# Optimization experiments

Hardware: AMD Instinct MI355X
Metric: run time of the kernel (lower is better)

Reference implementation:

```python
import jax, jax.numpy as jnp
import numpy as np

BATCH, T, VOCAB, HIDDEN = 32, 256, 8192, 1024
SCALE = 0.02  # small init so logits stay sane through the recurrence


def setup_inputs() -> dict:
    key = jax.random.key(0)
    ks = jax.random.split(key, 4)
    inputs = jax.random.normal(ks[0], (BATCH, T, VOCAB), dtype=jnp.float32)
    Wi = jax.random.normal(ks[1], (VOCAB, 4 * HIDDEN), dtype=jnp.float32) * SCALE
    Wh = jax.random.normal(ks[2], (HIDDEN, 4 * HIDDEN), dtype=jnp.float32) * SCALE
    bh = jnp.zeros((4 * HIDDEN,), dtype=jnp.float32)
    Wp = jax.random.normal(ks[3], (HIDDEN, VOCAB), dtype=jnp.float32) * SCALE
    bp = jnp.zeros((VOCAB,), dtype=jnp.float32)
    c0 = jnp.zeros((BATCH, HIDDEN), dtype=jnp.float32)
    h0 = jnp.zeros((BATCH, HIDDEN), dtype=jnp.float32)
    return {"inputs": inputs, "Wi": Wi, "Wh": Wh, "bh": bh,
            "Wp": Wp, "bp": bp, "c0": c0, "h0": h0}


def _decode(inputs, Wi, Wh, bh, Wp, bp, c0, h0, rng):
    vocab = inputs.shape[2]

    def step(carry, x_t):
        rng, c, h, last_pred = carry
        rng, cat_rng = jax.random.split(rng)
        x = last_pred  # teacher_force=False: feed back sampled one-hot token
        # fused LSTM gates (flax gate order i, f, g, o)
        z = x @ Wi + h @ Wh + bh  # [B, 4H]
        i, f, g, o = jnp.split(z, 4, axis=-1)
        c = jax.nn.sigmoid(f) * c + jax.nn.sigmoid(i) * jnp.tanh(g)
        h = jax.nn.sigmoid(o) * jnp.tanh(c)
        logits = h @ Wp + bp  # [B, V]
        tok = jax.random.categorical(cat_rng, logits)  # [B] int
        pred = jax.nn.one_hot(tok, vocab, dtype=jnp.float32)  # [B, V]
        return (rng, c, h, pred), (logits, pred)

    init = (rng, c0, h0, inputs[:, 0])
    xs = jnp.swapaxes(inputs, 0, 1)  # [T, B, V]
    _, (logits, preds) = jax.lax.scan(step, init, xs)
    # scan stacks on axis 0; original scan_in_dim puts time back on axis 1
    return jnp.swapaxes(logits, 0, 1), jnp.swapaxes(preds, 0, 1)


def reference(inputs, Wi, Wh, bh, Wp, bp, c0, h0):
    rng = jax.random.key(42)  # stands in for self.make_rng('lstm')
    return _decode(inputs, Wi, Wh, bh, Wp, bp, c0, h0, rng)
```

## Files before the change

### kernel.cpp

```cpp
#include <hip/hip_runtime.h>
#include <cstdint>
#include <cstddef>


namespace {

constexpr int BB = 32;
constexpr int TT = 256;
constexpr int VV = 8192;
constexpr int HH = 1024;
constexpr int ZC = 4096;
constexpr int NCOL = VV + ZC;
constexpr int SPL = 4;
constexpr int K0S = 8;

__host__ __device__ inline uint32_t rotl(uint32_t v, int r) {
  return (v << r) | (v >> (32 - r));
}

__host__ __device__ inline void tf2x32(uint32_t k0, uint32_t k1,
                                       uint32_t x0, uint32_t x1,
                                       uint32_t &o0, uint32_t &o1) {
  const uint32_t ks2 = k0 ^ k1 ^ 0x1BD11BDAu;
  x0 += k0; x1 += k1;
#define R4A { x0+=x1; x1=rotl(x1,13); x1^=x0; x0+=x1; x1=rotl(x1,15); x1^=x0; \
              x0+=x1; x1=rotl(x1,26); x1^=x0; x0+=x1; x1=rotl(x1, 6); x1^=x0; }
#define R4B { x0+=x1; x1=rotl(x1,17); x1^=x0; x0+=x1; x1=rotl(x1,29); x1^=x0; \
              x0+=x1; x1=rotl(x1,16); x1^=x0; x0+=x1; x1=rotl(x1,24); x1^=x0; }
  R4A; x0 += k1;  x1 += ks2 + 1u;
  R4B; x0 += ks2; x1 += k0 + 2u;
  R4A; x0 += k0;  x1 += k1 + 3u;
  R4B; x0 += k1;  x1 += ks2 + 4u;
  R4A; x0 += ks2; x1 += k0 + 5u;
#undef R4A
#undef R4B
  o0 = x0; o1 = x1;
}

__device__ inline float sigf(float x) { return 1.0f / (1.0f + expf(-x)); }

__global__ __launch_bounds__(256) void k0_partial(
    const float* __restrict__ inputs,
    const float* __restrict__ h0,
    const float* __restrict__ Wi,
    const float* __restrict__ Wh,
    float* __restrict__ zpart0)
{
  const int cb = blockIdx.x % (ZC / 64);
  const int s  = blockIdx.x / (ZC / 64);
  const int c  = threadIdx.x & 63;
  const int w  = threadIdx.x >> 6;
  const int col = cb * 64 + c;
  const int u0 = s * 1152 + w * 288;

  float acc[BB];
#pragma unroll
  for (int b = 0; b < BB; ++b) acc[b] = 0.0f;

  for (int ui = 0; ui < 288; ++ui) {
    const int u = u0 + ui;
    const float wv = (u < VV) ? Wi[(size_t)u * ZC + col]
                              : Wh[(size_t)(u - VV) * ZC + col];
#pragma unroll
    for (int b = 0; b < BB; ++b) {
      const float a = (u < VV) ? inputs[(size_t)b * TT * VV + u]
                               : h0[b * HH + (u - VV)];
      acc[b] = fmaf(a, wv, acc[b]);
    }
  }

  __shared__ float red[4][BB][64];
#pragma unroll
  for (int b = 0; b < BB; ++b) red[w][b][c] = acc[b];
  __syncthreads();
  for (int i = threadIdx.x; i < BB * 64; i += 256) {
    const int b = i >> 6, cc = i & 63;
    const float s4 = red[0][b][cc] + red[1][b][cc] + red[2][b][cc] + red[3][b][cc];
    zpart0[((size_t)s * BB + b) * ZC + cb * 64 + cc] = s4;
  }
}

__global__ __launch_bounds__(256) void k0_reduce(
    const float* __restrict__ zpart0, const float* __restrict__ bh,
    float* __restrict__ zfull0)
{
  const int idx = blockIdx.x * 256 + threadIdx.x;
  const int b = idx / ZC, j = idx % ZC;
  float s = bh[j];
#pragma unroll
  for (int k = 0; k < K0S; ++k) s += zpart0[((size_t)k * BB + b) * ZC + j];
  zfull0[idx] = s;
}

__global__ __launch_bounds__(256) void k1_cell(
    const float* __restrict__ part,
    const float* __restrict__ zfull0,
    const float* __restrict__ bh,
    const float* __restrict__ Wi,
    const float* __restrict__ c0,
    const float* __restrict__ argval,
    const int*   __restrict__ argidx,
    float* __restrict__ cbuf, float* __restrict__ hbuf,
    float* __restrict__ preds_out,
    int t)
{
  const int b = blockIdx.x;
  __shared__ int tok_sh;
  if (t > 0) {
    if (threadIdx.x < 64) {
      const int lane = threadIdx.x;
      float v = -3.4e38f; int idx = 0x7fffffff;
      if (lane < 32) { v = argval[b * 32 + lane]; idx = argidx[b * 32 + lane]; }
#pragma unroll
      for (int off = 16; off; off >>= 1) {
        const float vo = __shfl_down(v, off);
        const int   io = __shfl_down(idx, off);
        if (vo > v || (vo == v && io < idx)) { v = vo; idx = io; }
      }
      if (lane == 0) tok_sh = idx;
    }
    __syncthreads();
  }
  const int tok = (t > 0) ? tok_sh : 0;
  if (t > 0 && threadIdx.x == 0) {
    preds_out[((size_t)b * TT + (t - 1)) * VV + tok] = 1.0f;
  }

  for (int u = threadIdx.x; u < HH; u += 256) {
    float zi, zf, zg, zo;
    if (t == 0) {
      const float* z0 = zfull0 + (size_t)b * ZC;
      zi = z0[u]; zf = z0[HH + u]; zg = z0[2 * HH + u]; zo = z0[3 * HH + u];
    } else {
      zi = bh[u]; zf = bh[HH + u]; zg = bh[2 * HH + u]; zo = bh[3 * HH + u];
#pragma unroll
      for (int s = 0; s < SPL; ++s) {
        const float* p = part + ((size_t)s * BB + b) * NCOL + VV;
        zi += p[u]; zf += p[HH + u]; zg += p[2 * HH + u]; zo += p[3 * HH + u];
      }
      const float* wrow = Wi + (size_t)tok * ZC;
      zi += wrow[u]; zf += wrow[HH + u]; zg += wrow[2 * HH + u]; zo += wrow[3 * HH + u];
    }
    const float cprev = (t == 0) ? c0[b * HH + u] : cbuf[b * HH + u];
    const float cc = sigf(zf) * cprev + sigf(zi) * tanhf(zg);
    const float hh = sigf(zo) * tanhf(cc);
    cbuf[b * HH + u] = cc;
    hbuf[b * HH + u] = hh;
  }
}

__global__ __launch_bounds__(256) void k2_mm(
    const float* __restrict__ hbuf,
    const float* __restrict__ Wp,
    const float* __restrict__ Wh,
    float* __restrict__ part)
{
  const int cb = blockIdx.x % (NCOL / 64);
  const int s  = blockIdx.x / (NCOL / 64);
  const int c  = threadIdx.x & 63;
  const int w  = threadIdx.x >> 6;
  const int col = cb * 64 + c;

  const float* W; int ldw, wcol;
  if (col < VV) { W = Wp; ldw = VV; wcol = col; }
  else          { W = Wh; ldw = ZC; wcol = col - VV; }

  __shared__ float hs[BB][256];
  for (int i = threadIdx.x; i < BB * 256; i += 256) {
    const int b = i >> 8, uu = i & 255;
    hs[b][uu] = hbuf[b * HH + s * 256 + uu];
  }
  __syncthreads();

  float acc[BB];
#pragma unroll
  for (int b = 0; b < BB; ++b) acc[b] = 0.0f;

  const int ubase = w * 64;
  const float* wp = W + (size_t)(s * 256 + w * 64) * ldw + wcol;
  for (int uc = 0; uc < 8; ++uc) {
    float wv[8];
#pragma unroll
    for (int k = 0; k < 8; ++k) wv[k] = wp[(size_t)(uc * 8 + k) * ldw];
#pragma unroll
    for (int b = 0; b < BB; ++b) {
      const float4 h4a = *(const float4*)&hs[b][ubase + uc * 8];
      const float4 h4b = *(const float4*)&hs[b][ubase + uc * 8 + 4];
      acc[b] = fmaf(h4a.x, wv[0], acc[b]);
      acc[b] = fmaf(h4a.y, wv[1], acc[b]);
      acc[b] = fmaf(h4a.z, wv[2], acc[b]);
      acc[b] = fmaf(h4a.w, wv[3], acc[b]);
      acc[b] = fmaf(h4b.x, wv[4], acc[b]);
      acc[b] = fmaf(h4b.y, wv[5], acc[b]);
      acc[b] = fmaf(h4b.z, wv[6], acc[b]);
      acc[b] = fmaf(h4b.w, wv[7], acc[b]);
    }
  }

  __syncthreads();
  float* red = &hs[0][0];
#pragma unroll
  for (int b = 0; b < BB; ++b) red[(w * BB + b) * 64 + c] = acc[b];
  __syncthreads();
  for (int i = threadIdx.x; i < BB * 64; i += 256) {
    const int b = i >> 6, cc = i & 63;
    const float s4 = red[(0 * BB + b) * 64 + cc] + red[(1 * BB + b) * 64 + cc] +
                     red[(2 * BB + b) * 64 + cc] + red[(3 * BB + b) * 64 + cc];
    part[((size_t)s * BB + b) * NCOL + cb * 64 + cc] = s4;
  }
}

__global__ __launch_bounds__(256) void k3_logits(
    const float* __restrict__ part,
    const float* __restrict__ bp,
    float* __restrict__ logits_out,
    float* __restrict__ preds_out,
    float* __restrict__ argval, int* __restrict__ argidx,
    uint32_t ck0, uint32_t ck1, int t)
{
  const int b  = blockIdx.x >> 5;
  const int ch = blockIdx.x & 31;
  const int v  = ch * 256 + threadIdx.x;

  float lg = bp[v];
#pragma unroll
  for (int s = 0; s < SPL; ++s) lg += part[((size_t)s * BB + b) * NCOL + v];
  logits_out[((size_t)b * TT + t) * VV + v] = lg;
  preds_out [((size_t)b * TT + t) * VV + v] = 0.0f;

  const uint32_t j = (uint32_t)(b * VV + v);
  uint32_t r0, r1;
  tf2x32(ck0, ck1, 0u, j, r0, r1);
  const uint32_t bits = r0 ^ r1;
  const float u0 = __uint_as_float((bits >> 9) | 0x3f800000u) - 1.0f;
  const float uu = (u0 == 0.0f) ? 1.17549435e-38f : u0;
  const float g = -logf(-logf(uu));
  const float val = lg + g;

  __shared__ float sval[256];
  __shared__ int   sidx[256];
  sval[threadIdx.x] = val;
  sidx[threadIdx.x] = v;
  __syncthreads();
#pragma unroll
  for (int off = 128; off; off >>= 1) {
    if (threadIdx.x < off) {
      const float vo = sval[threadIdx.x + off];
      const int   io = sidx[threadIdx.x + off];
      if (vo > sval[threadIdx.x] ||
          (vo == sval[threadIdx.x] && io < sidx[threadIdx.x])) {
        sval[threadIdx.x] = vo; sidx[threadIdx.x] = io;
      }
    }
    __syncthreads();
  }
  if (threadIdx.x == 0) {
    argval[b * 32 + ch] = sval[0];
    argidx[b * 32 + ch] = sidx[0];
  }
}

__global__ __launch_bounds__(64) void kfinal(
    const float* __restrict__ argval, const int* __restrict__ argidx,
    float* __restrict__ preds_out)
{
  const int b = blockIdx.x, lane = threadIdx.x;
  float v = -3.4e38f; int idx = 0x7fffffff;
  if (lane < 32) { v = argval[b * 32 + lane]; idx = argidx[b * 32 + lane]; }
#pragma unroll
  for (int off = 16; off; off >>= 1) {
    const float vo = __shfl_down(v, off);
    const int   io = __shfl_down(idx, off);
    if (vo > v || (vo == v && io < idx)) { v = vo; idx = io; }
  }
  if (lane == 0) preds_out[((size_t)b * TT + (TT - 1)) * VV + idx] = 1.0f;
}

}

extern "C" void kernel_launch(void* const* d_in, const int* in_sizes, int n_in,
                              void* d_out, int out_size, void* d_ws, size_t ws_size,
                              hipStream_t stream) {
  const float* inputs = (const float*)d_in[0];
  const float* Wi     = (const float*)d_in[1];
  const float* Wh     = (const float*)d_in[2];
  const float* bh     = (const float*)d_in[3];
  const float* Wp     = (const float*)d_in[4];
  const float* bp     = (const float*)d_in[5];
  const float* c0     = (const float*)d_in[6];
  const float* h0     = (const float*)d_in[7];

  float* out_logits = (float*)d_out;
  float* out_preds  = out_logits + (size_t)BB * TT * VV;

  uint8_t* ws = (uint8_t*)d_ws;
  size_t off = 0;
  float* part   = (float*)(ws + off);
  float* zpart0 = (float*)(ws + off);
  off += (size_t)SPL * BB * NCOL * sizeof(float);
  float* zfull0 = (float*)(ws + off); off += (size_t)BB * ZC * sizeof(float);
  float* cbuf   = (float*)(ws + off); off += (size_t)BB * HH * sizeof(float);
  float* hbuf   = (float*)(ws + off); off += (size_t)BB * HH * sizeof(float);
  float* argval = (float*)(ws + off); off += (size_t)BB * 32 * sizeof(float);
  int*   argidx = (int*)  (ws + off); off += (size_t)BB * 32 * sizeof(int);

  uint32_t k0 = 0u, k1 = 42u;
  uint32_t ck[TT][2];
  for (int t = 0; t < TT; ++t) {
    uint32_t a, b2; tf2x32(k0, k1, 0u, 1u, a, b2);
    ck[t][0] = a; ck[t][1] = b2;
    uint32_t n0, n1; tf2x32(k0, k1, 0u, 0u, n0, n1);
    k0 = n0; k1 = n1;
  }

  k0_partial<<<(ZC / 64) * K0S, 256, 0, stream>>>(inputs, h0, Wi, Wh, zpart0);
  k0_reduce<<<BB * ZC / 256, 256, 0, stream>>>(zpart0, bh, zfull0);

  for (int t = 0; t < TT; ++t) {
    k1_cell<<<BB, 256, 0, stream>>>(part, zfull0, bh, Wi, c0, argval, argidx,
                                    cbuf, hbuf, out_preds, t);
    k2_mm<<<(NCOL / 64) * SPL, 256, 0, stream>>>(hbuf, Wp, Wh, part);
    k3_logits<<<BB * (VV / 256), 256, 0, stream>>>(part, bp, out_logits, out_preds,
                                                   argval, argidx, ck[t][0], ck[t][1], t);
  }
  kfinal<<<BB, 64, 0, stream>>>(argval, argidx, out_preds);
}
```

Measured before the change: 8.847 ms.

## Fuse logits, sampling argmax and LSTM cell into one per-batch kernel

Per-step launches drop from three to two. The logits/Gumbel-argmax kernel and the cell update are merged into a single 1024-thread block per batch row, which removes the cross-block argmax staging buffers and the final kernel. The matmul kernel stops staging h in shared memory and reads h directly from global memory, using readfirstlane to make it wave-uniform so the loads can be scalar. The cost is much lower parallelism in the fused kernel: only 32 blocks stream 8192 logits and preds per row.

```diff
diff --git a/kernel.cpp b/kernel.cpp
--- a/kernel.cpp
+++ b/kernel.cpp
@@ -92,64 +92,20 @@
   zfull0[idx] = s;
 }
 
-__global__ __launch_bounds__(256) void k1_cell(
-    const float* __restrict__ part,
-    const float* __restrict__ zfull0,
-    const float* __restrict__ bh,
-    const float* __restrict__ Wi,
-    const float* __restrict__ c0,
-    const float* __restrict__ argval,
-    const int*   __restrict__ argidx,
-    float* __restrict__ cbuf, float* __restrict__ hbuf,
-    float* __restrict__ preds_out,
-    int t)
-{
-  const int b = blockIdx.x;
-  __shared__ int tok_sh;
-  if (t > 0) {
-    if (threadIdx.x < 64) {
-      const int lane = threadIdx.x;
-      float v = -3.4e38f; int idx = 0x7fffffff;
-      if (lane < 32) { v = argval[b * 32 + lane]; idx = argidx[b * 32 + lane]; }
-#pragma unroll
-      for (int off = 16; off; off >>= 1) {
-        const float vo = __shfl_down(v, off);
-        const int   io = __shfl_down(idx, off);
-        if (vo > v || (vo == v && io < idx)) { v = vo; idx = io; }
-      }
-      if (lane == 0) tok_sh = idx;
-    }
-    __syncthreads();
-  }
-  const int tok = (t > 0) ? tok_sh : 0;
-  if (t > 0 && threadIdx.x == 0) {
-    preds_out[((size_t)b * TT + (t - 1)) * VV + tok] = 1.0f;
-  }
-
-  for (int u = threadIdx.x; u < HH; u += 256) {
-    float zi, zf, zg, zo;
-    if (t == 0) {
-      const float* z0 = zfull0 + (size_t)b * ZC;
-      zi = z0[u]; zf = z0[HH + u]; zg = z0[2 * HH + u]; zo = z0[3 * HH + u];
-    } else {
-      zi = bh[u]; zf = bh[HH + u]; zg = bh[2 * HH + u]; zo = bh[3 * HH + u];
-#pragma unroll
-      for (int s = 0; s < SPL; ++s) {
-        const float* p = part + ((size_t)s * BB + b) * NCOL + VV;
-        zi += p[u]; zf += p[HH + u]; zg += p[2 * HH + u]; zo += p[3 * HH + u];
-      }
-      const float* wrow = Wi + (size_t)tok * ZC;
-      zi += wrow[u]; zf += wrow[HH + u]; zg += wrow[2 * HH + u]; zo += wrow[3 * HH + u];
-    }
-    const float cprev = (t == 0) ? c0[b * HH + u] : cbuf[b * HH + u];
-    const float cc = sigf(zf) * cprev + sigf(zi) * tanhf(zg);
-    const float hh = sigf(zo) * tanhf(cc);
-    cbuf[b * HH + u] = cc;
-    hbuf[b * HH + u] = hh;
-  }
-}
-
-__global__ __launch_bounds__(256) void k2_mm(
+__global__ __launch_bounds__(256) void kInit(
+    const float* __restrict__ zfull0, const float* __restrict__ c0,
+    float* __restrict__ cbuf, float* __restrict__ hbuf)
+{
+  const int idx = blockIdx.x * 256 + threadIdx.x;
+  const int b = idx >> 10, u = idx & 1023;
+  const float* z = zfull0 + (size_t)b * ZC;
+  const float zi = z[u], zf = z[HH + u], zg = z[2 * HH + u], zo = z[3 * HH + u];
+  const float cc = sigf(zf) * c0[idx] + sigf(zi) * tanhf(zg);
+  cbuf[idx] = cc;
+  hbuf[idx] = sigf(zo) * tanhf(cc);
+}
+
+__global__ __launch_bounds__(256) void kA(
     const float* __restrict__ hbuf,
     const float* __restrict__ Wp,
     const float* __restrict__ Wh,
@@ -158,122 +114,122 @@
   const int cb = blockIdx.x % (NCOL / 64);
   const int s  = blockIdx.x / (NCOL / 64);
   const int c  = threadIdx.x & 63;
-  const int w  = threadIdx.x >> 6;
+  const int w  = __builtin_amdgcn_readfirstlane(threadIdx.x >> 6);
   const int col = cb * 64 + c;
 
   const float* W; int ldw, wcol;
   if (col < VV) { W = Wp; ldw = VV; wcol = col; }
   else          { W = Wh; ldw = ZC; wcol = col - VV; }
 
-  __shared__ float hs[BB][256];
-  for (int i = threadIdx.x; i < BB * 256; i += 256) {
-    const int b = i >> 8, uu = i & 255;
-    hs[b][uu] = hbuf[b * HH + s * 256 + uu];
-  }
-  __syncthreads();
+  const float* hb = hbuf + s * 256 + w * 64;
+  const float* wp = W + (size_t)(s * 256 + w * 64) * ldw + wcol;
 
   float acc[BB];
 #pragma unroll
   for (int b = 0; b < BB; ++b) acc[b] = 0.0f;
 
-  const int ubase = w * 64;
-  const float* wp = W + (size_t)(s * 256 + w * 64) * ldw + wcol;
   for (int uc = 0; uc < 8; ++uc) {
     float wv[8];
 #pragma unroll
     for (int k = 0; k < 8; ++k) wv[k] = wp[(size_t)(uc * 8 + k) * ldw];
 #pragma unroll
     for (int b = 0; b < BB; ++b) {
-      const float4 h4a = *(const float4*)&hs[b][ubase + uc * 8];
-      const float4 h4b = *(const float4*)&hs[b][ubase + uc * 8 + 4];
-      acc[b] = fmaf(h4a.x, wv[0], acc[b]);
-      acc[b] = fmaf(h4a.y, wv[1], acc[b]);
-      acc[b] = fmaf(h4a.z, wv[2], acc[b]);
-      acc[b] = fmaf(h4a.w, wv[3], acc[b]);
-      acc[b] = fmaf(h4b.x, wv[4], acc[b]);
-      acc[b] = fmaf(h4b.y, wv[5], acc[b]);
-      acc[b] = fmaf(h4b.z, wv[6], acc[b]);
-      acc[b] = fmaf(h4b.w, wv[7], acc[b]);
-    }
-  }
-
-  __syncthreads();
-  float* red = &hs[0][0];
-#pragma unroll
-  for (int b = 0; b < BB; ++b) red[(w * BB + b) * 64 + c] = acc[b];
+      const float* hp = hb + b * HH + uc * 8;
+      acc[b] = fmaf(hp[0], wv[0], acc[b]);
+      acc[b] = fmaf(hp[1], wv[1], acc[b]);
+      acc[b] = fmaf(hp[2], wv[2], acc[b]);
+      acc[b] = fmaf(hp[3], wv[3], acc[b]);
+      acc[b] = fmaf(hp[4], wv[4], acc[b]);
+      acc[b] = fmaf(hp[5], wv[5], acc[b]);
+      acc[b] = fmaf(hp[6], wv[6], acc[b]);
+      acc[b] = fmaf(hp[7], wv[7], acc[b]);
+    }
+  }
+
+  __shared__ float red[4][BB][64];
+#pragma unroll
+  for (int b = 0; b < BB; ++b) red[w][b][c] = acc[b];
   __syncthreads();
   for (int i = threadIdx.x; i < BB * 64; i += 256) {
     const int b = i >> 6, cc = i & 63;
-    const float s4 = red[(0 * BB + b) * 64 + cc] + red[(1 * BB + b) * 64 + cc] +
-                     red[(2 * BB + b) * 64 + cc] + red[(3 * BB + b) * 64 + cc];
+    const float s4 = red[0][b][cc] + red[1][b][cc] + red[2][b][cc] + red[3][b][cc];
     part[((size_t)s * BB + b) * NCOL + cb * 64 + cc] = s4;
   }
 }
 
-__global__ __launch_bounds__(256) void k3_logits(
+__global__ __launch_bounds__(1024) void kB(
     const float* __restrict__ part,
     const float* __restrict__ bp,
+    const float* __restrict__ bh,
+    const float* __restrict__ Wi,
     float* __restrict__ logits_out,
     float* __restrict__ preds_out,
-    float* __restrict__ argval, int* __restrict__ argidx,
-    uint32_t ck0, uint32_t ck1, int t)
-{
-  const int b  = blockIdx.x >> 5;
-  const int ch = blockIdx.x & 31;
-  const int v  = ch * 256 + threadIdx.x;
-
-  float lg = bp[v];
-#pragma unroll
-  for (int s = 0; s < SPL; ++s) lg += part[((size_t)s * BB + b) * NCOL + v];
-  logits_out[((size_t)b * TT + t) * VV + v] = lg;
-  preds_out [((size_t)b * TT + t) * VV + v] = 0.0f;
-
-  const uint32_t j = (uint32_t)(b * VV + v);
-  uint32_t r0, r1;
-  tf2x32(ck0, ck1, 0u, j, r0, r1);
-  const uint32_t bits = r0 ^ r1;
-  const float u0 = __uint_as_float((bits >> 9) | 0x3f800000u) - 1.0f;
-  const float uu = (u0 == 0.0f) ? 1.17549435e-38f : u0;
-  const float g = -logf(-logf(uu));
-  const float val = lg + g;
-
-  __shared__ float sval[256];
-  __shared__ int   sidx[256];
-  sval[threadIdx.x] = val;
-  sidx[threadIdx.x] = v;
-  __syncthreads();
-#pragma unroll
-  for (int off = 128; off; off >>= 1) {
-    if (threadIdx.x < off) {
-      const float vo = sval[threadIdx.x + off];
-      const int   io = sidx[threadIdx.x + off];
-      if (vo > sval[threadIdx.x] ||
-          (vo == sval[threadIdx.x] && io < sidx[threadIdx.x])) {
-        sval[threadIdx.x] = vo; sidx[threadIdx.x] = io;
-      }
-    }
-    __syncthreads();
-  }
-  if (threadIdx.x == 0) {
-    argval[b * 32 + ch] = sval[0];
-    argidx[b * 32 + ch] = sidx[0];
-  }
-}
-
-__global__ __launch_bounds__(64) void kfinal(
-    const float* __restrict__ argval, const int* __restrict__ argidx,
-    float* __restrict__ preds_out)
-{
-  const int b = blockIdx.x, lane = threadIdx.x;
-  float v = -3.4e38f; int idx = 0x7fffffff;
-  if (lane < 32) { v = argval[b * 32 + lane]; idx = argidx[b * 32 + lane]; }
-#pragma unroll
-  for (int off = 16; off; off >>= 1) {
-    const float vo = __shfl_down(v, off);
-    const int   io = __shfl_down(idx, off);
-    if (vo > v || (vo == v && io < idx)) { v = vo; idx = io; }
-  }
-  if (lane == 0) preds_out[((size_t)b * TT + (TT - 1)) * VV + idx] = 1.0f;
+    float* __restrict__ cbuf, float* __restrict__ hbuf,
+    uint32_t ck0, uint32_t ck1, int t, int do_cell)
+{
+  const int b = blockIdx.x;
+  const int tid = threadIdx.x;
+  float* lg_row = logits_out + ((size_t)b * TT + t) * VV;
+  float* pr_row = preds_out  + ((size_t)b * TT + t) * VV;
+
+  float best = -3.4e38f; int besti = 0x7fffffff;
+  for (int it = 0; it < VV / 1024; ++it) {
+    const int v = it * 1024 + tid;
+    float lg = bp[v];
+#pragma unroll
+    for (int s = 0; s < SPL; ++s) lg += part[((size_t)s * BB + b) * NCOL + v];
+    lg_row[v] = lg;
+    pr_row[v] = 0.0f;
+    uint32_t r0, r1;
+    tf2x32(ck0, ck1, 0u, (uint32_t)(b * VV + v), r0, r1);
+    const uint32_t bits = r0 ^ r1;
+    const float u0 = __uint_as_float((bits >> 9) | 0x3f800000u) - 1.0f;
+    const float uu = (u0 == 0.0f) ? 1.17549435e-38f : u0;
+    const float val = lg - logf(-logf(uu));
+    if (val > best) { best = val; besti = v; }
+  }
+#pragma unroll
+  for (int off = 32; off; off >>= 1) {
+    const float vo = __shfl_down(best, off);
+    const int   io = __shfl_down(besti, off);
+    if (vo > best || (vo == best && io < besti)) { best = vo; besti = io; }
+  }
+  __shared__ float wv_[16];
+  __shared__ int   wi_[16];
+  __shared__ int   stok;
+  const int wid = tid >> 6, lane = tid & 63;
+  if (lane == 0) { wv_[wid] = best; wi_[wid] = besti; }
+  __syncthreads();
+  if (tid < 64) {
+    float v2 = (lane < 16) ? wv_[lane] : -3.4e38f;
+    int   i2 = (lane < 16) ? wi_[lane] : 0x7fffffff;
+#pragma unroll
+    for (int off = 8; off; off >>= 1) {
+      const float vo = __shfl_down(v2, off);
+      const int   io = __shfl_down(i2, off);
+      if (vo > v2 || (vo == v2 && io < i2)) { v2 = vo; i2 = io; }
+    }
+    if (lane == 0) stok = i2;
+  }
+  __syncthreads();
+  const int tok = stok;
+  if (tid == 0) pr_row[tok] = 1.0f;
+
+  if (do_cell) {
+    const int u = tid;
+    float zi = bh[u], zf = bh[HH + u], zg = bh[2 * HH + u], zo = bh[3 * HH + u];
+#pragma unroll
+    for (int s = 0; s < SPL; ++s) {
+      const float* p = part + ((size_t)s * BB + b) * NCOL + VV;
+      zi += p[u]; zf += p[HH + u]; zg += p[2 * HH + u]; zo += p[3 * HH + u];
+    }
+    const float* wr = Wi + (size_t)tok * ZC;
+    zi += wr[u]; zf += wr[HH + u]; zg += wr[2 * HH + u]; zo += wr[3 * HH + u];
+    const float cp = cbuf[b * HH + u];
+    const float cc = sigf(zf) * cp + sigf(zi) * tanhf(zg);
+    cbuf[b * HH + u] = cc;
+    hbuf[b * HH + u] = sigf(zo) * tanhf(cc);
+  }
 }
 
 }
@@ -301,8 +257,6 @@
   float* zfull0 = (float*)(ws + off); off += (size_t)BB * ZC * sizeof(float);
   float* cbuf   = (float*)(ws + off); off += (size_t)BB * HH * sizeof(float);
   float* hbuf   = (float*)(ws + off); off += (size_t)BB * HH * sizeof(float);
-  float* argval = (float*)(ws + off); off += (size_t)BB * 32 * sizeof(float);
-  int*   argidx = (int*)  (ws + off); off += (size_t)BB * 32 * sizeof(int);
 
   uint32_t k0 = 0u, k1 = 42u;
   uint32_t ck[TT][2];
@@ -315,13 +269,12 @@
 
   k0_partial<<<(ZC / 64) * K0S, 256, 0, stream>>>(inputs, h0, Wi, Wh, zpart0);
   k0_reduce<<<BB * ZC / 256, 256, 0, stream>>>(zpart0, bh, zfull0);
+  kInit<<<BB * HH / 256, 256, 0, stream>>>(zfull0, c0, cbuf, hbuf);
 
   for (int t = 0; t < TT; ++t) {
-    k1_cell<<<BB, 256, 0, stream>>>(part, zfull0, bh, Wi, c0, argval, argidx,
-                                    cbuf, hbuf, out_preds, t);
-    k2_mm<<<(NCOL / 64) * SPL, 256, 0, stream>>>(hbuf, Wp, Wh, part);
-    k3_logits<<<BB * (VV / 256), 256, 0, stream>>>(part, bp, out_logits, out_preds,
-                                                   argval, argidx, ck[t][0], ck[t][1], t);
-  }
-  kfinal<<<BB, 64, 0, stream>>>(argval, argidx, out_preds);
-}
+    kA<<<(NCOL / 64) * SPL, 256, 0, stream>>>(hbuf, Wp, Wh, part);
+    kB<<<BB, 1024, 0, stream>>>(part, bp, bh, Wi, out_logits, out_preds,
+                                cbuf, hbuf, ck[t][0], ck[t][1], t,
+                                (t < TT - 1) ? 1 : 0);
+  }
+}
```

New measurement: 15.91 ms. 1.8x slower.

## Retile recurrent matmul with 4-column float4 register blocking and deeper K-split

Applied to the files above, without the earlier changes.

The per-step h @ [Wp|Wh] kernel is restructured. Each thread now computes 4 adjacent columns for 16 batch rows using float4 weight loads, and the K dimension is split across wave pairs inside a block. When workspace allows, the split count rises from 4 to 8 to raise block count. The goals are more reuse of each LDS h value, wider vectorised weight reads, and more parallelism across the small batch. The cost is more partial sums for the downstream reductions to read, plus higher register pressure under a 2-blocks-per-CU launch bound.

```diff
diff --git a/kernel.cpp b/kernel.cpp
--- a/kernel.cpp
+++ b/kernel.cpp
@@ -11,7 +11,6 @@
 constexpr int HH = 1024;
 constexpr int ZC = 4096;
 constexpr int NCOL = VV + ZC;
-constexpr int SPL = 4;
 constexpr int K0S = 8;
 
 __host__ __device__ inline uint32_t rotl(uint32_t v, int r) {
@@ -92,6 +91,7 @@
   zfull0[idx] = s;
 }
 
+template <int SPL>
 __global__ __launch_bounds__(256) void k1_cell(
     const float* __restrict__ part,
     const float* __restrict__ zfull0,
@@ -149,67 +149,103 @@
   }
 }
 
-__global__ __launch_bounds__(256) void k2_mm(
+template <int SPL>
+__global__ __launch_bounds__(256, 2) void kA(
     const float* __restrict__ hbuf,
     const float* __restrict__ Wp,
     const float* __restrict__ Wh,
     float* __restrict__ part)
 {
-  const int cb = blockIdx.x % (NCOL / 64);
-  const int s  = blockIdx.x / (NCOL / 64);
-  const int c  = threadIdx.x & 63;
-  const int w  = threadIdx.x >> 6;
-  const int col = cb * 64 + c;
-
-  const float* W; int ldw, wcol;
-  if (col < VV) { W = Wp; ldw = VV; wcol = col; }
-  else          { W = Wh; ldw = ZC; wcol = col - VV; }
-
-  __shared__ float hs[BB][256];
-  for (int i = threadIdx.x; i < BB * 256; i += 256) {
-    const int b = i >> 8, uu = i & 255;
-    hs[b][uu] = hbuf[b * HH + s * 256 + uu];
+  constexpr int UB  = HH / SPL;
+  constexpr int UWH = UB / 2;
+  constexpr int UC  = UWH / 8;
+  constexpr int NCB = NCOL / 256;
+
+  const int cb    = blockIdx.x % NCB;
+  const int s     = blockIdx.x / NCB;
+  const int lane  = threadIdx.x & 63;
+  const int w     = threadIdx.x >> 6;
+  const int uhalf = w >> 1;
+  const int bhalf = w & 1;
+  const int b0    = bhalf * 16;
+  const int colbase = cb * 256;
+
+  const float* W; int ldw, wcol0;
+  if (colbase < VV) { W = Wp; ldw = VV; wcol0 = colbase + lane * 4; }
+  else              { W = Wh; ldw = ZC; wcol0 = colbase - VV + lane * 4; }
+
+  __shared__ __align__(16) float smem[BB * UB];
+
+  const int u0 = s * UB;
+  for (int f = threadIdx.x * 4; f < BB * UB; f += 1024) {
+    const int b = f / UB, uu = f % UB;
+    *(float4*)&smem[b * UB + uu] = *(const float4*)&hbuf[b * HH + u0 + uu];
   }
   __syncthreads();
 
-  float acc[BB];
-#pragma unroll
-  for (int b = 0; b < BB; ++b) acc[b] = 0.0f;
-
-  const int ubase = w * 64;
-  const float* wp = W + (size_t)(s * 256 + w * 64) * ldw + wcol;
-  for (int uc = 0; uc < 8; ++uc) {
-    float wv[8];
-#pragma unroll
-    for (int k = 0; k < 8; ++k) wv[k] = wp[(size_t)(uc * 8 + k) * ldw];
-#pragma unroll
-    for (int b = 0; b < BB; ++b) {
-      const float4 h4a = *(const float4*)&hs[b][ubase + uc * 8];
-      const float4 h4b = *(const float4*)&hs[b][ubase + uc * 8 + 4];
-      acc[b] = fmaf(h4a.x, wv[0], acc[b]);
-      acc[b] = fmaf(h4a.y, wv[1], acc[b]);
-      acc[b] = fmaf(h4a.z, wv[2], acc[b]);
-      acc[b] = fmaf(h4a.w, wv[3], acc[b]);
-      acc[b] = fmaf(h4b.x, wv[4], acc[b]);
-      acc[b] = fmaf(h4b.y, wv[5], acc[b]);
-      acc[b] = fmaf(h4b.z, wv[6], acc[b]);
-      acc[b] = fmaf(h4b.w, wv[7], acc[b]);
-    }
-  }
-
-  __syncthreads();
-  float* red = &hs[0][0];
-#pragma unroll
-  for (int b = 0; b < BB; ++b) red[(w * BB + b) * 64 + c] = acc[b];
-  __syncthreads();
-  for (int i = threadIdx.x; i < BB * 64; i += 256) {
-    const int b = i >> 6, cc = i & 63;
-    const float s4 = red[(0 * BB + b) * 64 + cc] + red[(1 * BB + b) * 64 + cc] +
-                     red[(2 * BB + b) * 64 + cc] + red[(3 * BB + b) * 64 + cc];
-    part[((size_t)s * BB + b) * NCOL + cb * 64 + cc] = s4;
-  }
-}
-
+  float4 acc[16];
+#pragma unroll
+  for (int i = 0; i < 16; ++i) acc[i] = make_float4(0.f, 0.f, 0.f, 0.f);
+
+  const int uloc0 = uhalf * UWH;
+  const float* wp = W + (size_t)(u0 + uloc0) * ldw + wcol0;
+
+#pragma unroll 1
+  for (int uc = 0; uc < UC; ++uc) {
+    float4 wv[8];
+#pragma unroll
+    for (int k = 0; k < 8; ++k)
+      wv[k] = *(const float4*)&wp[(size_t)(uc * 8 + k) * ldw];
+#pragma unroll
+    for (int bl = 0; bl < 16; ++bl) {
+      const float* hrow = &smem[(b0 + bl) * UB + uloc0 + uc * 8];
+      const float4 ha = *(const float4*)&hrow[0];
+      const float4 hb = *(const float4*)&hrow[4];
+      float4 a = acc[bl];
+      a.x = fmaf(wv[0].x, ha.x, a.x); a.y = fmaf(wv[0].y, ha.x, a.y);
+      a.z = fmaf(wv[0].z, ha.x, a.z); a.w = fmaf(wv[0].w, ha.x, a.w);
+      a.x = fmaf(wv[1].x, ha.y, a.x); a.y = fmaf(wv[1].y, ha.y, a.y);
+      a.z = fmaf(wv[1].z, ha.y, a.z); a.w = fmaf(wv[1].w, ha.y, a.w);
+      a.x = fmaf(wv[2].x, ha.z, a.x); a.y = fmaf(wv[2].y, ha.z, a.y);
+      a.z = fmaf(wv[2].z, ha.z, a.z); a.w = fmaf(wv[2].w, ha.z, a.w);
+      a.x = fmaf(wv[3].x, ha.w, a.x); a.y = fmaf(wv[3].y, ha.w, a.y);
+      a.z = fmaf(wv[3].z, ha.w, a.z); a.w = fmaf(wv[3].w, ha.w, a.w);
+      a.x = fmaf(wv[4].x, hb.x, a.x); a.y = fmaf(wv[4].y, hb.x, a.y);
+      a.z = fmaf(wv[4].z, hb.x, a.z); a.w = fmaf(wv[4].w, hb.x, a.w);
+      a.x = fmaf(wv[5].x, hb.y, a.x); a.y = fmaf(wv[5].y, hb.y, a.y);
+      a.z = fmaf(wv[5].z, hb.y, a.z); a.w = fmaf(wv[5].w, hb.y, a.w);
+      a.x = fmaf(wv[6].x, hb.z, a.x); a.y = fmaf(wv[6].y, hb.z, a.y);
+      a.z = fmaf(wv[6].z, hb.z, a.z); a.w = fmaf(wv[6].w, hb.z, a.w);
+      a.x = fmaf(wv[7].x, hb.w, a.x); a.y = fmaf(wv[7].y, hb.w, a.y);
+      a.z = fmaf(wv[7].z, hb.w, a.z); a.w = fmaf(wv[7].w, hb.w, a.w);
+      acc[bl] = a;
+    }
+  }
+
+  float4* red = (float4*)smem;
+#pragma unroll
+  for (int rb = 0; rb < 4; ++rb) {
+    __syncthreads();
+#pragma unroll
+    for (int bl = 0; bl < 4; ++bl)
+      red[((bhalf * 2 + uhalf) * 4 + bl) * 64 + lane] = acc[rb * 4 + bl];
+    __syncthreads();
+#pragma unroll
+    for (int rep = 0; rep < 2; ++rep) {
+      const int i  = rep * 256 + threadIdx.x;
+      const int ln = i & 63, bl = (i >> 6) & 3, bh2 = i >> 8;
+      const float4 r0 = red[((bh2 * 2 + 0) * 4 + bl) * 64 + ln];
+      const float4 r1 = red[((bh2 * 2 + 1) * 4 + bl) * 64 + ln];
+      float4 o;
+      o.x = r0.x + r1.x; o.y = r0.y + r1.y;
+      o.z = r0.z + r1.z; o.w = r0.w + r1.w;
+      const int b = bh2 * 16 + rb * 4 + bl;
+      *(float4*)&part[((size_t)s * BB + b) * NCOL + colbase + ln * 4] = o;
+    }
+  }
+}
+
+template <int SPL>
 __global__ __launch_bounds__(256) void k3_logits(
     const float* __restrict__ part,
     const float* __restrict__ bp,
@@ -293,11 +329,16 @@
   float* out_logits = (float*)d_out;
   float* out_preds  = out_logits + (size_t)BB * TT * VV;
 
+  const size_t partB8 = (size_t)8 * BB * NCOL * sizeof(float);
+  const size_t tailB  = ((size_t)BB * ZC + (size_t)BB * HH * 2 +
+                         (size_t)BB * 32 * 2) * sizeof(float);
+  const int spl = (ws_size >= partB8 + tailB + 1024) ? 8 : 4;
+  const size_t partB = (size_t)spl * BB * NCOL * sizeof(float);
+
   uint8_t* ws = (uint8_t*)d_ws;
-  size_t off = 0;
-  float* part   = (float*)(ws + off);
-  float* zpart0 = (float*)(ws + off);
-  off += (size_t)SPL * BB * NCOL * sizeof(float);
+  float* part   = (float*)ws;
+  float* zpart0 = (float*)ws;
+  size_t off = partB;
   float* zfull0 = (float*)(ws + off); off += (size_t)BB * ZC * sizeof(float);
   float* cbuf   = (float*)(ws + off); off += (size_t)BB * HH * sizeof(float);
   float* hbuf   = (float*)(ws + off); off += (size_t)BB * HH * sizeof(float);
@@ -317,11 +358,19 @@
   k0_reduce<<<BB * ZC / 256, 256, 0, stream>>>(zpart0, bh, zfull0);
 
   for (int t = 0; t < TT; ++t) {
-    k1_cell<<<BB, 256, 0, stream>>>(part, zfull0, bh, Wi, c0, argval, argidx,
-                                    cbuf, hbuf, out_preds, t);
-    k2_mm<<<(NCOL / 64) * SPL, 256, 0, stream>>>(hbuf, Wp, Wh, part);
-    k3_logits<<<BB * (VV / 256), 256, 0, stream>>>(part, bp, out_logits, out_preds,
-                                                   argval, argidx, ck[t][0], ck[t][1], t);
+    if (spl == 8) {
+      k1_cell<8><<<BB, 256, 0, stream>>>(part, zfull0, bh, Wi, c0, argval,
+                                         argidx, cbuf, hbuf, out_preds, t);
+      kA<8><<<(NCOL / 256) * 8, 256, 0, stream>>>(hbuf, Wp, Wh, part);
+      k3_logits<8><<<BB * 32, 256, 0, stream>>>(part, bp, out_logits, out_preds,
+                                                argval, argidx, ck[t][0], ck[t][1], t);
+    } else {
+      k1_cell<4><<<BB, 256, 0, stream>>>(part, zfull0, bh, Wi, c0, argval,
+                                         argidx, cbuf, hbuf, out_preds, t);
+      kA<4><<<(NCOL / 256) * 4, 256, 0, stream>>>(hbuf, Wp, Wh, part);
+      k3_logits<4><<<BB * 32, 256, 0, stream>>>(part, bp, out_logits, out_preds,
+                                                argval, argidx, ck[t][0], ck[t][1], t);
+    }
   }
   kfinal<<<BB, 64, 0, stream>>>(argval, argidx, out_preds);
 }
```

Result: slower. 10.80 ms (+22.1%).
